# Kernel optimization log

Measured on AMD Instinct MI355X. Metric: run time of the kernel, lower is better.

## Reference

```python
import jax, jax.numpy as jnp
import numpy as np

D = 1024  # in_features == latent_dim
EPS = 1e-5


def _layernorm(x, g, b):
    mu = jnp.mean(x, axis=-1, keepdims=True)
    var = jnp.mean(jnp.square(x - mu), axis=-1, keepdims=True)
    return (x - mu) * jax.lax.rsqrt(var + EPS) * g + b


def setup_inputs() -> dict:
    key = jax.random.key(0)
    ks = jax.random.split(key, 8)
    s = 1.0 / np.sqrt(D)
    return {
        "x": jax.random.normal(ks[0], (4, 4096, D), dtype=jnp.float32),
        "w_qkv": jax.random.uniform(ks[1], (3 * D, D), jnp.float32, -s, s),
        "w_o": jax.random.uniform(ks[2], (D, D), jnp.float32, -s, s),
        "w1": jax.random.uniform(ks[3], (D, D), jnp.float32, -s, s),
        "b1": jax.random.uniform(ks[4], (D,), jnp.float32, -s, s),
        "w2": jax.random.uniform(ks[5], (D, D), jnp.float32, -s, s),
        "b2": jax.random.uniform(ks[6], (D,), jnp.float32, -s, s),
        "ln1_g": jnp.ones((D,), jnp.float32),
        "ln1_b": jnp.zeros((D,), jnp.float32),
        "ln2_g": jnp.ones((D,), jnp.float32),
        "ln2_b": jnp.zeros((D,), jnp.float32),
    }


def reference(x, w_qkv, w_o, w1, b1, w2, b2, ln1_g, ln1_b, ln2_g, ln2_b):
    B, S, _ = x.shape
    scale = 1.0 / np.sqrt(D * 1)  # 1/sqrt(latent_dim * n_heads), n_heads=1
    qkv = jnp.einsum("bsd,ed->bse", x, w_qkv)            # [B,S,3D]
    qkv = qkv.reshape(B, S, 1, 3 * D).transpose(0, 2, 1, 3)  # [B,1,S,3D]
    q, k, v = jnp.split(qkv, 3, axis=-1)                  # each [B,1,S,D]
    logits = jnp.einsum("bhid,bhjd->bhij", q, k) * scale  # [B,1,S,S]
    # Faithful quirk: softmax over the HEAD axis (dim=1). With 1 head this
    # yields an all-ones attention matrix.
    attn = jax.nn.softmax(logits, axis=1)
    vals = jnp.einsum("bhij,bhjd->bhid", attn, v)         # [B,1,S,D]
    vals = vals.transpose(0, 2, 1, 3).reshape(B, S, D)
    attn_out = jnp.einsum("bsd,ed->bse", vals, w_o)
    # squeeze(-2) is a no-op for S>1
    x = _layernorm(x + attn_out, ln1_g, ln1_b)
    h = jax.nn.gelu(jnp.einsum("bsd,ed->bse", x, w1) + b1, approximate=False)
    mlp_out = jnp.einsum("bsd,ed->bse", h, w2) + b2
    return _layernorm(x + mlp_out, ln2_g, ln2_b)
```

## Files before the change

### kernel.cpp

```cpp
#include <hip/hip_runtime.h>
#include <hip/hip_bf16.h>

typedef __hip_bfloat16 bf16;
typedef __attribute__((ext_vector_type(8))) short short8;
typedef __attribute__((ext_vector_type(4))) float f32x4;

#define DDIM 1024
#define SEQ  4096
#define NB   4
#define MTOT (NB*SEQ)

static __device__ __forceinline__ unsigned short f2bf(float f) {
    __hip_bfloat16 h = __float2bfloat16(f);
    unsigned short u; __builtin_memcpy(&u, &h, 2); return u;
}
static __device__ __forceinline__ float bf2f(unsigned short u) {
    __hip_bfloat16 h; __builtin_memcpy(&h, &u, 2); return __bfloat162float(h);
}

__global__ __launch_bounds__(256) void cast_w_kernel(
    const float* __restrict__ w1, const float* __restrict__ w2,
    unsigned short* __restrict__ w1b, unsigned short* __restrict__ w2b)
{
    size_t idx = ((size_t)blockIdx.x*256 + threadIdx.x) * 4;
    float4 a = *(const float4*)(w1 + idx);
    ushort4 o; o.x=f2bf(a.x); o.y=f2bf(a.y); o.z=f2bf(a.z); o.w=f2bf(a.w);
    *(ushort4*)(w1b + idx) = o;
    float4 b = *(const float4*)(w2 + idx);
    o.x=f2bf(b.x); o.y=f2bf(b.y); o.z=f2bf(b.z); o.w=f2bf(b.w);
    *(ushort4*)(w2b + idx) = o;
}

__global__ __launch_bounds__(256) void colsum_partial_kernel(
    const float* __restrict__ x, float* __restrict__ partial)
{
    int d  = blockIdx.x*256 + threadIdx.x;
    int b  = blockIdx.y;
    int sl = blockIdx.z;
    const float* p = x + ((size_t)b*SEQ + (size_t)sl*128)*DDIM + d;
    float s = 0.f;
    #pragma unroll 4
    for (int i = 0; i < 128; ++i) s += p[(size_t)i*DDIM];
    partial[((size_t)sl*NB + b)*DDIM + d] = s;
}

__global__ __launch_bounds__(256) void colsum_reduce_kernel(
    const float* __restrict__ partial, float* __restrict__ xsum)
{
    int d = blockIdx.x*256 + threadIdx.x;
    int b = blockIdx.y;
    float s = 0.f;
    #pragma unroll
    for (int sl = 0; sl < 32; ++sl) s += partial[((size_t)sl*NB + b)*DDIM + d];
    xsum[b*DDIM + d] = s;
}

__global__ __launch_bounds__(256) void matvec_kernel(
    const float* __restrict__ W, const float* __restrict__ vin, float* __restrict__ vout)
{
    int b = blockIdx.y;
    int g = threadIdx.x >> 4;
    int t = threadIdx.x & 15;
    int e = blockIdx.x*16 + g;
    const float* w = W + (size_t)e*DDIM;
    const float* v = vin + b*DDIM;
    float s = 0.f;
    for (int k = t; k < DDIM; k += 16) s += w[k]*v[k];
    #pragma unroll
    for (int o = 8; o; o >>= 1) s += __shfl_down(s, o, 16);
    if (t == 0) vout[b*DDIM + e] = s;
}

__global__ __launch_bounds__(256) void ln1_kernel(
    const float* __restrict__ x, const float* __restrict__ avec,
    const float* __restrict__ g1, const float* __restrict__ b1,
    unsigned short* __restrict__ x1b)
{
    int row = blockIdx.x;
    int b   = row >> 12;
    int tid = threadIdx.x;
    const float4* xr = (const float4*)(x + (size_t)row*DDIM);
    const float4* av = (const float4*)(avec + (size_t)b*DDIM);
    float4 xv = xr[tid], a4 = av[tid];
    float y0 = xv.x+a4.x, y1 = xv.y+a4.y, y2 = xv.z+a4.z, y3 = xv.w+a4.w;
    float s  = y0+y1+y2+y3;
    float ss = y0*y0+y1*y1+y2*y2+y3*y3;
    #pragma unroll
    for (int o = 32; o; o >>= 1) { s += __shfl_down(s,o,64); ss += __shfl_down(ss,o,64); }
    __shared__ float red[8];
    if ((tid&63) == 0) { red[tid>>6] = s; red[4+(tid>>6)] = ss; }
    __syncthreads();
    float St = red[0]+red[1]+red[2]+red[3];
    float Sq = red[4]+red[5]+red[6]+red[7];
    float mu = St*(1.0f/DDIM);
    float rs = rsqrtf(Sq*(1.0f/DDIM) - mu*mu + 1e-5f);
    float4 g4 = ((const float4*)g1)[tid];
    float4 bb = ((const float4*)b1)[tid];
    ushort4 o;
    o.x = f2bf((y0-mu)*rs*g4.x + bb.x);
    o.y = f2bf((y1-mu)*rs*g4.y + bb.y);
    o.z = f2bf((y2-mu)*rs*g4.z + bb.z);
    o.w = f2bf((y3-mu)*rs*g4.w + bb.w);
    *(ushort4*)(x1b + (size_t)row*DDIM + tid*4) = o;
}

__global__ __launch_bounds__(512, 1) void gemm8p_kernel(
    const bf16* __restrict__ A, const bf16* __restrict__ Bw,
    const float* __restrict__ bias, unsigned short* __restrict__ outb)
{
    extern __shared__ char smem[];
    const int tid  = threadIdx.x;
    const int wave = tid >> 6, lane = tid & 63;

    int bid = blockIdx.x;
    int swz = (bid & 7) * 32 + (bid >> 3);
    const size_t bm = (size_t)(swz >> 2) * 256;
    const size_t bn = (size_t)(swz & 3) * 256;

    const int wm = wave >> 2;
    const int wn = wave & 3;

    const int srow = tid >> 3;
    const int skel = (((tid & 7) ^ ((tid >> 3) & 7)) << 3);
    const int fr = lane & 15, fs = lane >> 4;

    const bf16* Ab = A  + bm * 1024;
    const bf16* Bb = Bw + bn * 1024;

#define REGN(d,mat,h) (smem + ((((d)<<2)|((mat)<<1)|(h))<<14))
#define STAGE(dst, srcb, kt) { \
    _Pragma("unroll") for (int g_ = 0; g_ < 2; ++g_) { \
        const bf16* gp_ = (srcb) + (size_t)(g_*64 + srow)*1024 + (kt)*64 + skel; \
        __builtin_amdgcn_global_load_lds( \
            (const __attribute__((address_space(1))) void*)gp_, \
            (__attribute__((address_space(3))) void*)((dst) + g_*8192 + wave*1024), \
            16, 0, 0); } }
#define RDA(d,kk,dst) { const char* ba_ = REGN(d,0,wm); \
    _Pragma("unroll") for (int mf_ = 0; mf_ < 8; ++mf_) { \
        int lr_ = mf_*16 + fr; int ph_ = ((kk)*4 + fs) ^ (lr_ & 7); \
        dst[mf_] = *(const short8*)(ba_ + lr_*128 + ph_*16); } }
#define RDB(d,kk,dst) { const char* bb_ = REGN(d,1,(wn>>1)); \
    _Pragma("unroll") for (int nf_ = 0; nf_ < 4; ++nf_) { \
        int lr_ = (wn&1)*64 + nf_*16 + fr; int ph_ = ((kk)*4 + fs) ^ (lr_ & 7); \
        dst[nf_] = *(const short8*)(bb_ + lr_*128 + ph_*16); } }
#define MM(AF,BF,NB_) { __builtin_amdgcn_s_setprio(1); \
    _Pragma("unroll") for (int mf_ = 0; mf_ < 8; ++mf_) \
        _Pragma("unroll") for (int nn_ = 0; nn_ < 2; ++nn_) \
            acc[mf_][(NB_)+nn_] = __builtin_amdgcn_mfma_f32_16x16x32_bf16( \
                AF[mf_], BF[(NB_)+nn_], acc[mf_][(NB_)+nn_], 0, 0, 0); \
    __builtin_amdgcn_s_setprio(0); }
#define BAR  __builtin_amdgcn_s_barrier()
#define LGK0 asm volatile("s_waitcnt lgkmcnt(0)" ::: "memory")
#define LGK8 asm volatile("s_waitcnt lgkmcnt(8)" ::: "memory")
#define VM4  asm volatile("s_waitcnt vmcnt(4)"  ::: "memory")
#define VM0  asm volatile("s_waitcnt vmcnt(0)"  ::: "memory")

    short8 a0[8], a1[8], b0[4], b1[4];
    f32x4 acc[8][4] = {};

    STAGE(REGN(0,0,0), Ab,          0); STAGE(REGN(0,0,1), Ab + 128*1024, 0);
    STAGE(REGN(0,1,0), Bb,          0); STAGE(REGN(0,1,1), Bb + 128*1024, 0);
    STAGE(REGN(1,0,0), Ab,          1); STAGE(REGN(1,0,1), Ab + 128*1024, 1);
    VM4;
    BAR;

    for (int j = 0; j < 8; ++j) {
        const int k1 = 2*j + 1, k2 = 2*j + 2, k3 = 2*j + 3;
        const bool t2 = (k2 < 16), t3 = (k3 < 16);
        RDA(0,0,a0); RDB(0,0,b0);
        STAGE(REGN(1,1,0), Bb, k1);
        LGK8;
        BAR; LGK0; MM(a0,b0,0); BAR;
        RDA(0,1,a1);
        STAGE(REGN(1,1,1), Bb + 128*1024, k1);
        BAR; LGK0; MM(a0,b0,2); BAR;
        RDB(0,1,b1);
        if (t2) STAGE(REGN(0,0,0), Ab, k2);
        BAR; LGK0; MM(a1,b1,0); BAR;
        if (t2) { STAGE(REGN(0,0,1), Ab + 128*1024, k2); VM4; } else { VM0; }
        BAR; LGK0; MM(a1,b1,2); BAR;
        RDA(1,0,a0); RDB(1,0,b0);
        if (t2) STAGE(REGN(0,1,0), Bb, k2);
        LGK8;
        BAR; LGK0; MM(a0,b0,0); BAR;
        RDA(1,1,a1);
        if (t2) STAGE(REGN(0,1,1), Bb + 128*1024, k2);
        BAR; LGK0; MM(a0,b0,2); BAR;
        RDB(1,1,b1);
        if (t3) STAGE(REGN(1,0,0), Ab, k3);
        BAR; LGK0; MM(a1,b1,0); BAR;
        if (t3) { STAGE(REGN(1,0,1), Ab + 128*1024, k3); VM4; }
        BAR; LGK0; MM(a1,b1,2); BAR;
    }

    #pragma unroll
    for (int nf = 0; nf < 4; ++nf) {
        size_t col = bn + wn*64 + nf*16 + fr;
        float bv = bias[col];
        #pragma unroll
        for (int mf = 0; mf < 8; ++mf) {
            #pragma unroll
            for (int rr = 0; rr < 4; ++rr) {
                size_t row = bm + wm*128 + mf*16 + fs*4 + rr;
                float v = acc[mf][nf][rr] + bv;
                float ge = 0.5f*v*(1.0f + erff(v*0.70710678118f));
                outb[row*1024 + col] = f2bf(ge);
            }
        }
    }
#undef REGN
#undef STAGE
#undef RDA
#undef RDB
#undef MM
#undef BAR
#undef LGK0
#undef LGK8
#undef VM4
#undef VM0
}

__global__ __launch_bounds__(256, 2) void gemm2_kernel(
    const bf16* __restrict__ A, const bf16* __restrict__ Bw,
    const float* __restrict__ bias, unsigned short* __restrict__ xy,
    float2* __restrict__ part)
{
    constexpr int K = 1024, N = 1024, BK = 64, NT = K / BK;
    __shared__ __align__(16) bf16 lds[2][2][128*BK];
    const int tid  = threadIdx.x;
    const int wave = tid >> 6, lane = tid & 63;

    int bid = blockIdx.x;
    int swz = (bid & 7) * 128 + (bid >> 3);
    const size_t bm = (size_t)(swz >> 3) * 128;
    const size_t bn = (size_t)(swz & 7) * 128;

    const int wm = wave >> 1;
    const int wn = wave & 1;

    const int srow = tid >> 3;
    const int skel = (((tid & 7) ^ ((tid >> 3) & 7)) << 3);

    const int fr = lane & 15;
    const int fs = lane >> 4;
    int foff[2];
    #pragma unroll
    for (int ks = 0; ks < 2; ++ks)
        foff[ks] = fr*128 + (((ks*4 + fs) ^ (fr & 7)) << 4);

    f32x4 acc[4][4] = {};
    const bf16* Ab = A  + bm * K;
    const bf16* Bb = Bw + bn * K;

    auto stage = [&](int b, int kt) {
        #pragma unroll
        for (int mat = 0; mat < 2; ++mat) {
            const bf16* src = (mat == 0 ? Ab : Bb);
            #pragma unroll
            for (int g = 0; g < 4; ++g) {
                int row = g*32 + srow;
                const bf16* gp = src + (size_t)row * K + kt*BK + skel;
                __builtin_amdgcn_global_load_lds(
                    (const __attribute__((address_space(1))) void*)gp,
                    (__attribute__((address_space(3))) void*)
                        ((char*)&lds[b][mat][0] + g*4096 + wave*1024),
                    16, 0, 0);
            }
        }
    };

    stage(0, 0);

    #pragma unroll 2
    for (int t = 0; t < NT; ++t) {
        const int cur = t & 1;
        if (t < NT-1) {
            stage(cur ^ 1, t + 1);
            asm volatile("s_waitcnt vmcnt(8)" ::: "memory");
        } else {
            asm volatile("s_waitcnt vmcnt(0)" ::: "memory");
        }
        __builtin_amdgcn_s_barrier();

        const char* LA = (const char*)&lds[cur][0][0] + wm*8192;
        const char* LB = (const char*)&lds[cur][1][0] + wn*8192;
        #pragma unroll
        for (int ks = 0; ks < 2; ++ks) {
            short8 af[4], bfr[4];
            #pragma unroll
            for (int m = 0; m < 4; ++m) af[m]  = *(const short8*)(LA + m*2048 + foff[ks]);
            #pragma unroll
            for (int n = 0; n < 4; ++n) bfr[n] = *(const short8*)(LB + n*2048 + foff[ks]);
            __builtin_amdgcn_s_setprio(1);
            #pragma unroll
            for (int m = 0; m < 4; ++m)
                #pragma unroll
                for (int n = 0; n < 4; ++n)
                    acc[m][n] = __builtin_amdgcn_mfma_f32_16x16x32_bf16(
                        af[m], bfr[n], acc[m][n], 0, 0, 0);
            __builtin_amdgcn_s_setprio(0);
        }
        __builtin_amdgcn_s_barrier();
    }

    float vs[4][4] = {}, vq[4][4] = {};
    #pragma unroll
    for (int n = 0; n < 4; ++n) {
        size_t col = bn + wn*64 + n*16 + fr;
        float bv = bias[col];
        #pragma unroll
        for (int m = 0; m < 4; ++m) {
            #pragma unroll
            for (int r = 0; r < 4; ++r) {
                size_t row = bm + wm*64 + m*16 + fs*4 + r;
                size_t idx = row*(size_t)N + col;
                float v = acc[m][n][r] + bv + bf2f(xy[idx]);
                unsigned short qb = f2bf(v);
                xy[idx] = qb;
                float vv = bf2f(qb);
                vs[m][r] += vv;
                vq[m][r] += vv*vv;
            }
        }
    }
    #pragma unroll
    for (int o = 1; o < 16; o <<= 1) {
        #pragma unroll
        for (int m = 0; m < 4; ++m)
            #pragma unroll
            for (int r = 0; r < 4; ++r) {
                vs[m][r] += __shfl_xor(vs[m][r], o);
                vq[m][r] += __shfl_xor(vq[m][r], o);
            }
    }
    float* lred = (float*)&lds[0][0][0];
    if (fr == 0) {
        #pragma unroll
        for (int m = 0; m < 4; ++m)
            #pragma unroll
            for (int r = 0; r < 4; ++r) {
                int rl = wm*64 + m*16 + fs*4 + r;
                lred[(wn*128 + rl)*2]     = vs[m][r];
                lred[(wn*128 + rl)*2 + 1] = vq[m][r];
            }
    }
    __syncthreads();
    if (tid < 128) {
        float s  = lred[tid*2]       + lred[(128 + tid)*2];
        float sq = lred[tid*2 + 1]   + lred[(128 + tid)*2 + 1];
        part[(bm + tid)*8 + (bn >> 7)] = make_float2(s, sq);
    }
}

__global__ __launch_bounds__(256) void ln2_apply_kernel(
    const unsigned short* __restrict__ yb, const float2* __restrict__ part,
    const float* __restrict__ g2, const float* __restrict__ b2,
    float* __restrict__ out)
{
    int row = blockIdx.x;
    int tid = threadIdx.x;
    float s = 0.f, sq = 0.f;
    #pragma unroll
    for (int i = 0; i < 8; ++i) {
        float2 p = part[(size_t)row*8 + i];
        s += p.x; sq += p.y;
    }
    float mu = s * (1.0f/DDIM);
    float rs = rsqrtf(sq * (1.0f/DDIM) - mu*mu + 1e-5f);
    ushort4 yv = *(const ushort4*)(yb + (size_t)row*DDIM + tid*4);
    float4 g4 = ((const float4*)g2)[tid];
    float4 bb = ((const float4*)b2)[tid];
    float4 o;
    o.x = (bf2f(yv.x) - mu)*rs*g4.x + bb.x;
    o.y = (bf2f(yv.y) - mu)*rs*g4.y + bb.y;
    o.z = (bf2f(yv.z) - mu)*rs*g4.z + bb.z;
    o.w = (bf2f(yv.w) - mu)*rs*g4.w + bb.w;
    ((float4*)(out + (size_t)row*DDIM))[tid] = o;
}

extern "C" void kernel_launch(void* const* d_in, const int* in_sizes, int n_in,
                              void* d_out, int out_size, void* d_ws, size_t ws_size,
                              hipStream_t stream)
{
    const float* x     = (const float*)d_in[0];
    const float* w_qkv = (const float*)d_in[1];
    const float* w_o   = (const float*)d_in[2];
    const float* w1    = (const float*)d_in[3];
    const float* b1    = (const float*)d_in[4];
    const float* w2    = (const float*)d_in[5];
    const float* b2    = (const float*)d_in[6];
    const float* ln1g  = (const float*)d_in[7];
    const float* ln1b  = (const float*)d_in[8];
    const float* ln2g  = (const float*)d_in[9];
    const float* ln2b  = (const float*)d_in[10];
    float* out = (float*)d_out;
    char* ws = (char*)d_ws;

    unsigned short* x1b = (unsigned short*)(ws);
    unsigned short* hb  = (unsigned short*)(ws + 33554432);
    unsigned short* w1b = (unsigned short*)(ws + 67108864);
    unsigned short* w2b = (unsigned short*)(ws + 69206016);
    float* partial = (float*)(ws + 71303168);
    float* xsum    = (float*)(ws + 71827456);
    float* tvec    = (float*)(ws + 71843840);
    float* avec    = (float*)(ws + 71860224);
    float2* lnpart = (float2*)(ws + 67108864);

    (void)hipFuncSetAttribute((const void*)gemm8p_kernel,
                              hipFuncAttributeMaxDynamicSharedMemorySize, 131072);

    cast_w_kernel<<<dim3(1024), 256, 0, stream>>>(w1, w2, w1b, w2b);
    colsum_partial_kernel<<<dim3(4, NB, 32), 256, 0, stream>>>(x, partial);
    colsum_reduce_kernel<<<dim3(4, NB), 256, 0, stream>>>(partial, xsum);
    matvec_kernel<<<dim3(64, NB), 256, 0, stream>>>(w_qkv + (size_t)2*DDIM*DDIM, xsum, tvec);
    matvec_kernel<<<dim3(64, NB), 256, 0, stream>>>(w_o, tvec, avec);
    ln1_kernel<<<dim3(MTOT), 256, 0, stream>>>(x, avec, ln1g, ln1b, x1b);
    gemm8p_kernel<<<dim3(256), 512, 131072, stream>>>(
        (const bf16*)x1b, (const bf16*)w1b, b1, hb);
    gemm2_kernel<<<dim3(1024), 256, 0, stream>>>(
        (const bf16*)hb, (const bf16*)w2b, b2, x1b, lnpart);
    ln2_apply_kernel<<<dim3(MTOT), 256, 0, stream>>>(x1b, lnpart, ln2g, ln2b, out);
}
```

Before: 171.6 us.

## Fuse prep kernels, shrink GEMM1 fragment registers, use tanh GELU

Merges the weight cast and column-sum partial kernels into one launch and folds the partial reduction into the first matvec through shared memory, removing two launches. GEMM1 now keeps only one A fragment set and two B fragments at a time, re-reading B more often, and requests two blocks per CU in its launch bounds. The erf-based GELU epilogue is replaced by the tanh approximation using a fast exponential. This trades accuracy against the exact GELU, and the occupancy hint may not be realisable given the 128KB dynamic LDS per block.

```diff
diff --git a/kernel.cpp b/kernel.cpp
--- a/kernel.cpp
+++ b/kernel.cpp
@@ -18,41 +18,56 @@
     __hip_bfloat16 h; __builtin_memcpy(&h, &u, 2); return __bfloat162float(h);
 }
 
-__global__ __launch_bounds__(256) void cast_w_kernel(
+__global__ __launch_bounds__(256) void prep_kernel(
     const float* __restrict__ w1, const float* __restrict__ w2,
-    unsigned short* __restrict__ w1b, unsigned short* __restrict__ w2b)
-{
-    size_t idx = ((size_t)blockIdx.x*256 + threadIdx.x) * 4;
-    float4 a = *(const float4*)(w1 + idx);
-    ushort4 o; o.x=f2bf(a.x); o.y=f2bf(a.y); o.z=f2bf(a.z); o.w=f2bf(a.w);
-    *(ushort4*)(w1b + idx) = o;
-    float4 b = *(const float4*)(w2 + idx);
-    o.x=f2bf(b.x); o.y=f2bf(b.y); o.z=f2bf(b.z); o.w=f2bf(b.w);
-    *(ushort4*)(w2b + idx) = o;
-}
-
-__global__ __launch_bounds__(256) void colsum_partial_kernel(
+    unsigned short* __restrict__ w1b, unsigned short* __restrict__ w2b,
     const float* __restrict__ x, float* __restrict__ partial)
 {
-    int d  = blockIdx.x*256 + threadIdx.x;
-    int b  = blockIdx.y;
-    int sl = blockIdx.z;
-    const float* p = x + ((size_t)b*SEQ + (size_t)sl*128)*DDIM + d;
+    int bid = blockIdx.x;
+    if (bid < 1024) {
+        size_t idx = ((size_t)bid*256 + threadIdx.x) * 4;
+        float4 a = *(const float4*)(w1 + idx);
+        ushort4 o; o.x=f2bf(a.x); o.y=f2bf(a.y); o.z=f2bf(a.z); o.w=f2bf(a.w);
+        *(ushort4*)(w1b + idx) = o;
+        float4 b = *(const float4*)(w2 + idx);
+        o.x=f2bf(b.x); o.y=f2bf(b.y); o.z=f2bf(b.z); o.w=f2bf(b.w);
+        *(ushort4*)(w2b + idx) = o;
+    } else {
+        int idx = bid - 1024;
+        int dx = idx & 3, b = (idx >> 2) & 3, sl = idx >> 4;
+        int d  = dx*256 + threadIdx.x;
+        const float* p = x + ((size_t)b*SEQ + (size_t)sl*128)*DDIM + d;
+        float s = 0.f;
+        #pragma unroll 4
+        for (int i = 0; i < 128; ++i) s += p[(size_t)i*DDIM];
+        partial[((size_t)sl*NB + b)*DDIM + d] = s;
+    }
+}
+
+__global__ __launch_bounds__(256) void matvec1_kernel(
+    const float* __restrict__ W, const float* __restrict__ partial,
+    float* __restrict__ vout)
+{
+    int b = blockIdx.y;
+    __shared__ float vloc[DDIM];
+    #pragma unroll
+    for (int j = 0; j < 4; ++j) {
+        int d = j*256 + threadIdx.x;
+        float s = 0.f;
+        #pragma unroll
+        for (int sl = 0; sl < 32; ++sl) s += partial[((size_t)sl*NB + b)*DDIM + d];
+        vloc[d] = s;
+    }
+    __syncthreads();
+    int g = threadIdx.x >> 4;
+    int t = threadIdx.x & 15;
+    int e = blockIdx.x*16 + g;
+    const float* w = W + (size_t)e*DDIM;
     float s = 0.f;
-    #pragma unroll 4
-    for (int i = 0; i < 128; ++i) s += p[(size_t)i*DDIM];
-    partial[((size_t)sl*NB + b)*DDIM + d] = s;
-}
-
-__global__ __launch_bounds__(256) void colsum_reduce_kernel(
-    const float* __restrict__ partial, float* __restrict__ xsum)
-{
-    int d = blockIdx.x*256 + threadIdx.x;
-    int b = blockIdx.y;
-    float s = 0.f;
-    #pragma unroll
-    for (int sl = 0; sl < 32; ++sl) s += partial[((size_t)sl*NB + b)*DDIM + d];
-    xsum[b*DDIM + d] = s;
+    for (int k = t; k < DDIM; k += 16) s += w[k]*vloc[k];
+    #pragma unroll
+    for (int o = 8; o; o >>= 1) s += __shfl_down(s, o, 16);
+    if (t == 0) vout[b*DDIM + e] = s;
 }
 
 __global__ __launch_bounds__(256) void matvec_kernel(
@@ -104,7 +119,7 @@
     *(ushort4*)(x1b + (size_t)row*DDIM + tid*4) = o;
 }
 
-__global__ __launch_bounds__(512, 1) void gemm8p_kernel(
+__global__ __launch_bounds__(512, 2) void gemm1_8p_kernel(
     const bf16* __restrict__ A, const bf16* __restrict__ Bw,
     const float* __restrict__ bias, unsigned short* __restrict__ outb)
 {
@@ -135,27 +150,26 @@
             (const __attribute__((address_space(1))) void*)gp_, \
             (__attribute__((address_space(3))) void*)((dst) + g_*8192 + wave*1024), \
             16, 0, 0); } }
-#define RDA(d,kk,dst) { const char* ba_ = REGN(d,0,wm); \
+#define RDA(d,kk) { const char* ba_ = REGN(d,0,wm); \
     _Pragma("unroll") for (int mf_ = 0; mf_ < 8; ++mf_) { \
         int lr_ = mf_*16 + fr; int ph_ = ((kk)*4 + fs) ^ (lr_ & 7); \
-        dst[mf_] = *(const short8*)(ba_ + lr_*128 + ph_*16); } }
-#define RDB(d,kk,dst) { const char* bb_ = REGN(d,1,(wn>>1)); \
-    _Pragma("unroll") for (int nf_ = 0; nf_ < 4; ++nf_) { \
-        int lr_ = (wn&1)*64 + nf_*16 + fr; int ph_ = ((kk)*4 + fs) ^ (lr_ & 7); \
-        dst[nf_] = *(const short8*)(bb_ + lr_*128 + ph_*16); } }
-#define MM(AF,BF,NB_) { __builtin_amdgcn_s_setprio(1); \
+        a[mf_] = *(const short8*)(ba_ + lr_*128 + ph_*16); } }
+#define RDB2(d,kk,nh) { const char* bb_ = REGN(d,1,(wn>>1)); \
+    _Pragma("unroll") for (int nn_ = 0; nn_ < 2; ++nn_) { \
+        int lr_ = (wn&1)*64 + ((nh)*2+nn_)*16 + fr; int ph_ = ((kk)*4 + fs) ^ (lr_ & 7); \
+        b[nn_] = *(const short8*)(bb_ + lr_*128 + ph_*16); } }
+#define MM2(nbase) { __builtin_amdgcn_s_setprio(1); \
     _Pragma("unroll") for (int mf_ = 0; mf_ < 8; ++mf_) \
         _Pragma("unroll") for (int nn_ = 0; nn_ < 2; ++nn_) \
-            acc[mf_][(NB_)+nn_] = __builtin_amdgcn_mfma_f32_16x16x32_bf16( \
-                AF[mf_], BF[(NB_)+nn_], acc[mf_][(NB_)+nn_], 0, 0, 0); \
+            acc[mf_][(nbase)+nn_] = __builtin_amdgcn_mfma_f32_16x16x32_bf16( \
+                a[mf_], b[nn_], acc[mf_][(nbase)+nn_], 0, 0, 0); \
     __builtin_amdgcn_s_setprio(0); }
 #define BAR  __builtin_amdgcn_s_barrier()
 #define LGK0 asm volatile("s_waitcnt lgkmcnt(0)" ::: "memory")
-#define LGK8 asm volatile("s_waitcnt lgkmcnt(8)" ::: "memory")
 #define VM4  asm volatile("s_waitcnt vmcnt(4)"  ::: "memory")
 #define VM0  asm volatile("s_waitcnt vmcnt(0)"  ::: "memory")
 
-    short8 a0[8], a1[8], b0[4], b1[4];
+    short8 a[8], b[2];
     f32x4 acc[8][4] = {};
 
     STAGE(REGN(0,0,0), Ab,          0); STAGE(REGN(0,0,1), Ab + 128*1024, 0);
@@ -167,30 +181,30 @@
     for (int j = 0; j < 8; ++j) {
         const int k1 = 2*j + 1, k2 = 2*j + 2, k3 = 2*j + 3;
         const bool t2 = (k2 < 16), t3 = (k3 < 16);
-        RDA(0,0,a0); RDB(0,0,b0);
+        RDA(0,0); RDB2(0,0,0);
         STAGE(REGN(1,1,0), Bb, k1);
-        LGK8;
-        BAR; LGK0; MM(a0,b0,0); BAR;
-        RDA(0,1,a1);
+        BAR; LGK0; MM2(0); BAR;
+        RDB2(0,0,1);
         STAGE(REGN(1,1,1), Bb + 128*1024, k1);
-        BAR; LGK0; MM(a0,b0,2); BAR;
-        RDB(0,1,b1);
+        BAR; LGK0; MM2(2); BAR;
+        RDA(0,1); RDB2(0,1,0);
         if (t2) STAGE(REGN(0,0,0), Ab, k2);
-        BAR; LGK0; MM(a1,b1,0); BAR;
+        BAR; LGK0; MM2(0); BAR;
+        RDB2(0,1,1);
         if (t2) { STAGE(REGN(0,0,1), Ab + 128*1024, k2); VM4; } else { VM0; }
-        BAR; LGK0; MM(a1,b1,2); BAR;
-        RDA(1,0,a0); RDB(1,0,b0);
+        BAR; LGK0; MM2(2); BAR;
+        RDA(1,0); RDB2(1,0,0);
         if (t2) STAGE(REGN(0,1,0), Bb, k2);
-        LGK8;
-        BAR; LGK0; MM(a0,b0,0); BAR;
-        RDA(1,1,a1);
+        BAR; LGK0; MM2(0); BAR;
+        RDB2(1,0,1);
         if (t2) STAGE(REGN(0,1,1), Bb + 128*1024, k2);
-        BAR; LGK0; MM(a0,b0,2); BAR;
-        RDB(1,1,b1);
+        BAR; LGK0; MM2(2); BAR;
+        RDA(1,1); RDB2(1,1,0);
         if (t3) STAGE(REGN(1,0,0), Ab, k3);
-        BAR; LGK0; MM(a1,b1,0); BAR;
+        BAR; LGK0; MM2(0); BAR;
+        RDB2(1,1,1);
         if (t3) { STAGE(REGN(1,0,1), Ab + 128*1024, k3); VM4; }
-        BAR; LGK0; MM(a1,b1,2); BAR;
+        BAR; LGK0; MM2(2); BAR;
     }
 
     #pragma unroll
@@ -203,7 +217,9 @@
             for (int rr = 0; rr < 4; ++rr) {
                 size_t row = bm + wm*128 + mf*16 + fs*4 + rr;
                 float v = acc[mf][nf][rr] + bv;
-                float ge = 0.5f*v*(1.0f + erff(v*0.70710678118f));
+                float u = 0.7978845608f * (v + 0.044715f*v*v*v);
+                float e = __expf(2.0f*u);
+                float ge = 0.5f*v*(1.0f + (1.0f - 2.0f/(e + 1.0f)));
                 outb[row*1024 + col] = f2bf(ge);
             }
         }
@@ -211,11 +227,10 @@
 #undef REGN
 #undef STAGE
 #undef RDA
-#undef RDB
-#undef MM
+#undef RDB2
+#undef MM2
 #undef BAR
 #undef LGK0
-#undef LGK8
 #undef VM4
 #undef VM0
 }
@@ -401,21 +416,19 @@
     unsigned short* w1b = (unsigned short*)(ws + 67108864);
     unsigned short* w2b = (unsigned short*)(ws + 69206016);
     float* partial = (float*)(ws + 71303168);
-    float* xsum    = (float*)(ws + 71827456);
     float* tvec    = (float*)(ws + 71843840);
     float* avec    = (float*)(ws + 71860224);
     float2* lnpart = (float2*)(ws + 67108864);
 
-    (void)hipFuncSetAttribute((const void*)gemm8p_kernel,
+    (void)hipFuncSetAttribute((const void*)gemm1_8p_kernel,
                               hipFuncAttributeMaxDynamicSharedMemorySize, 131072);
 
-    cast_w_kernel<<<dim3(1024), 256, 0, stream>>>(w1, w2, w1b, w2b);
-    colsum_partial_kernel<<<dim3(4, NB, 32), 256, 0, stream>>>(x, partial);
-    colsum_reduce_kernel<<<dim3(4, NB), 256, 0, stream>>>(partial, xsum);
-    matvec_kernel<<<dim3(64, NB), 256, 0, stream>>>(w_qkv + (size_t)2*DDIM*DDIM, xsum, tvec);
+    prep_kernel<<<dim3(1536), 256, 0, stream>>>(w1, w2, w1b, w2b, x, partial);
+    matvec1_kernel<<<dim3(64, NB), 256, 0, stream>>>(
+        w_qkv + (size_t)2*DDIM*DDIM, partial, tvec);
     matvec_kernel<<<dim3(64, NB), 256, 0, stream>>>(w_o, tvec, avec);
     ln1_kernel<<<dim3(MTOT), 256, 0, stream>>>(x, avec, ln1g, ln1b, x1b);
-    gemm8p_kernel<<<dim3(256), 512, 131072, stream>>>(
+    gemm1_8p_kernel<<<dim3(256), 512, 131072, stream>>>(
         (const bf16*)x1b, (const bf16*)w1b, b1, hb);
     gemm2_kernel<<<dim3(1024), 256, 0, stream>>>(
         (const bf16*)hb, (const bf16*)w2b, b2, x1b, lnpart);
```

After: 165.7 us. 3.4% less time.
